# Optimization experiments

Hardware: AMD Instinct MI355X
Metric: run time of the kernel (lower is better)

Reference implementation:

```python
import jax, jax.numpy as jnp
import numpy as np

B, S, HID = 1, 2048, 2048
NH = 16
QL, KVL = 1536, 512
DN, DR, DV = 128, 64, 128
DQ = DN + DR  # 192
IH, ID = 4, 128
TOPK = 1024
EPS = 1e-6
THETA = 10000.0


def rope_interleaved(x, cos, sin):
    # x: (b,s,h,d); cos/sin: (s,d//2); pairs are (x[...,2i], x[...,2i+1])
    xr = x[..., 0::2]
    xi = x[..., 1::2]
    c = cos[None, :, None, :]
    s = sin[None, :, None, :]
    yr = xr * c - xi * s
    yi = xr * s + xi * c
    return jnp.stack([yr, yi], axis=-1).reshape(x.shape)


def rope_noninterleaved(x, cos, sin):
    # rotate-half style: pairs are (x[...,i], x[...,i+d/2])
    d = x.shape[-1] // 2
    x1, x2 = x[..., :d], x[..., d:]
    c = cos[None, :, None, :]
    s = sin[None, :, None, :]
    return jnp.concatenate([x1 * c - x2 * s, x1 * s + x2 * c], axis=-1)


def rmsnorm(x, w):
    var = jnp.mean(x * x, axis=-1, keepdims=True)
    return w * (x * jax.lax.rsqrt(var + EPS))


def layernorm(x, g, b):
    mu = jnp.mean(x, axis=-1, keepdims=True)
    var = jnp.mean((x - mu) ** 2, axis=-1, keepdims=True)
    return (x - mu) * jax.lax.rsqrt(var + EPS) * g + b


def setup_inputs() -> dict:
    key = jax.random.key(0)
    ks = jax.random.split(key, 12)
    std = 0.02
    x = jax.random.normal(ks[0], (B, S, HID), jnp.float32)
    pos = jnp.arange(S, dtype=jnp.float32)
    inv_freq = THETA ** (-jnp.arange(0, DR, 2, dtype=jnp.float32) / DR)
    ang = pos[:, None] * inv_freq[None, :]  # (S, DR//2)
    cos, sin = jnp.cos(ang), jnp.sin(ang)
    mask = jnp.where(jnp.tril(jnp.ones((S, S), bool)), 0.0, -1e9).astype(jnp.float32)
    return {
        "x": x, "cos": cos, "sin": sin, "mask": mask,
        "Wq_a": jax.random.normal(ks[1], (HID, QL), jnp.float32) * std,
        "q_norm_w": jnp.ones((QL,), jnp.float32),
        "Wq_b": jax.random.normal(ks[2], (QL, NH * DQ), jnp.float32) * std,
        "Wkv_a": jax.random.normal(ks[3], (HID, KVL + DR), jnp.float32) * std,
        "kv_norm_w": jnp.ones((KVL,), jnp.float32),
        "Wkv_b": jax.random.normal(ks[4], (KVL, NH * (DN + DV)), jnp.float32) * std,
        "Wo": jax.random.normal(ks[5], (NH * DV, HID), jnp.float32) * std,
        "IWq_b": jax.random.normal(ks[6], (QL, IH * ID), jnp.float32) * std,
        "IWk": jax.random.normal(ks[7], (HID, ID), jnp.float32) * std,
        "Ik_norm_w": jnp.ones((ID,), jnp.float32),
        "Ik_norm_b": jnp.zeros((ID,), jnp.float32),
        "IWproj": jax.random.normal(ks[8], (HID, IH), jnp.float32) * std,
    }


def indexer(x, qr, cos, sin, mask, IWq_b, IWk, Ik_norm_w, Ik_norm_b, IWproj):
    b, s, _ = x.shape
    q = (qr @ IWq_b).reshape(b, s, IH, ID)
    q_pe, q_nope = q[..., :DR], q[..., DR:]
    q_pe = rope_noninterleaved(q_pe, cos, sin)
    q = jnp.concatenate([q_pe, q_nope], axis=-1)
    k = layernorm(x @ IWk, Ik_norm_w, Ik_norm_b)  # (b,s,ID)
    k_pe = rope_noninterleaved(k[:, :, None, :DR], cos, sin)[:, :, 0]
    k = jnp.concatenate([k_pe, k[..., DR:]], axis=-1)
    weights = (x @ IWproj) * (IH ** -0.5) * (ID ** -0.5)  # (b,s,IH)
    logits = jax.nn.relu(jnp.einsum('bthd,bsd->btsh', q, k))
    index_score = jnp.einsum('btsh,bth->bts', logits, weights)
    index_score = index_score + mask[None]
    k_top = min(TOPK, s)
    topk_idx = jax.lax.top_k(index_score, k_top)[1]  # (b,s,k)
    bi = jnp.arange(b)[:, None, None]
    si = jnp.arange(s)[None, :, None]
    index_mask = jnp.full((b, s, s), -1e9, jnp.float32).at[bi, si, topk_idx].set(0.0)
    return index_mask


def reference(x, cos, sin, mask, Wq_a, q_norm_w, Wq_b, Wkv_a, kv_norm_w, Wkv_b, Wo,
              IWq_b, IWk, Ik_norm_w, Ik_norm_b, IWproj):
    b, s, _ = x.shape
    qr = rmsnorm(x @ Wq_a, q_norm_w)  # (b,s,QL)
    q = (qr @ Wq_b).reshape(b, s, NH, DQ)
    q_nope, q_pe = q[..., :DN], q[..., DN:]
    q_pe = rope_interleaved(q_pe, cos, sin)
    q = jnp.concatenate([q_nope, q_pe], axis=-1)
    kv_full = x @ Wkv_a
    kv, k_pe = kv_full[..., :KVL], kv_full[..., KVL:]
    kv = rmsnorm(kv, kv_norm_w)
    k_pe = rope_interleaved(k_pe[:, :, None, :], cos, sin)  # (b,s,1,DR)
    kv_exp = (kv @ Wkv_b).reshape(b, s, NH, DN + DV)
    k_nope, v = kv_exp[..., :DN], kv_exp[..., DN:]
    k = jnp.concatenate([k_nope, jnp.broadcast_to(k_pe, (b, s, NH, DR))], axis=-1)
    scores = jnp.einsum('bshd,bthd->bsht', q, k) * (DQ ** -0.5)
    index_mask = indexer(x, qr, cos, sin, mask, IWq_b, IWk, Ik_norm_w, Ik_norm_b, IWproj)
    scores = scores + index_mask[:, :, None, :] + mask[None, :, None, :]
    probs = jax.nn.softmax(scores, axis=-1)
    out = jnp.einsum('bsht,bthd->bshd', probs, v).reshape(b, s, NH * DV)
    return out @ Wo
```

## Files before the change

### kernel.cpp

```cpp
#include <hip/hip_runtime.h>
#include <math.h>
#include <stdint.h>

#define S 2048
#define HID 2048
#define NH 16
#define QL 1536
#define KVL 512
#define DN 128
#define DR 64
#define DV 128
#define DQ 192
#define IH 4
#define ID 128
#define TOPK 1024

#define N1 2244
#define N2 3584

#define CDIV(a,b) (((a)+(b)-1)/(b))

typedef float f32x4 __attribute__((ext_vector_type(4)));
typedef short bf16x8 __attribute__((ext_vector_type(8)));

__device__ __forceinline__ ushort f2b(float f) {
    uint32_t u = __float_as_uint(f);
    u += 0x7fffu + ((u >> 16) & 1u);
    return (ushort)(u >> 16);
}

#define GLL16(g, l)                                                            \
    __builtin_amdgcn_global_load_lds(                                          \
        (const __attribute__((address_space(1))) void*)(g),                    \
        (__attribute__((address_space(3))) void*)(l), 16, 0, 0)

__global__ __launch_bounds__(256) void gemm_bt(const ushort* __restrict__ A,
                                               const ushort* __restrict__ BT,
                                               float* __restrict__ C,
                                               int M, int N, int K) {
    __shared__ ushort As[2][128 * 32];
    __shared__ ushort Bs[2][128 * 32];
    const int tid = threadIdx.x;
    const int w = tid >> 6, l = tid & 63;
    const int quad = l >> 4, lane = l & 15;
    const int row0 = blockIdx.y * 128, col0 = blockIdx.x * 128;
    const int wr = (w >> 1) * 64, wc = (w & 1) * 64;
    f32x4 acc[4][4];
#pragma unroll
    for (int i = 0; i < 4; i++)
#pragma unroll
        for (int j = 0; j < 4; j++) acc[i][j] = (f32x4)0.f;

    const int srow = w * 32 + (l >> 2);
    const int c8 = (l & 3) * 8;
    const ushort* pa0 = A + (size_t)(row0 + srow) * K + c8;
    const ushort* pa1 = A + (size_t)(row0 + srow + 16) * K + c8;
    int bn0 = col0 + srow;      if (bn0 > N - 1) bn0 = N - 1;
    int bn1 = col0 + srow + 16; if (bn1 > N - 1) bn1 = N - 1;
    const ushort* pb0 = BT + (size_t)bn0 * K + c8;
    const ushort* pb1 = BT + (size_t)bn1 * K + c8;
    const int soff = srow * 32 + c8;

    GLL16(pa0, &As[0][soff]);
    GLL16(pa1, &As[0][soff + 16 * 32]);
    GLL16(pb0, &Bs[0][soff]);
    GLL16(pb1, &Bs[0][soff + 16 * 32]);
    asm volatile("s_waitcnt vmcnt(0)" ::: "memory");
    __builtin_amdgcn_s_barrier();

    int cur = 0;
    for (int k0 = 0; k0 < K; k0 += 32) {
        const int nxt = cur ^ 1;
        if (k0 + 32 < K) {
            GLL16(pa0 + k0 + 32, &As[nxt][soff]);
            GLL16(pa1 + k0 + 32, &As[nxt][soff + 16 * 32]);
            GLL16(pb0 + k0 + 32, &Bs[nxt][soff]);
            GLL16(pb1 + k0 + 32, &Bs[nxt][soff + 16 * 32]);
        }
        bf16x8 af[4], bf[4];
#pragma unroll
        for (int mi = 0; mi < 4; mi++)
            af[mi] = *(const bf16x8*)(&As[cur][(wr + mi * 16 + lane) * 32 + quad * 8]);
#pragma unroll
        for (int ni = 0; ni < 4; ni++)
            bf[ni] = *(const bf16x8*)(&Bs[cur][(wc + ni * 16 + lane) * 32 + quad * 8]);
#pragma unroll
        for (int mi = 0; mi < 4; mi++)
#pragma unroll
            for (int ni = 0; ni < 4; ni++)
                acc[mi][ni] = __builtin_amdgcn_mfma_f32_16x16x32_bf16(af[mi], bf[ni], acc[mi][ni], 0, 0, 0);
        asm volatile("s_waitcnt vmcnt(0)" ::: "memory");
        __builtin_amdgcn_s_barrier();
        cur = nxt;
    }
#pragma unroll
    for (int mi = 0; mi < 4; mi++)
#pragma unroll
        for (int ni = 0; ni < 4; ni++)
#pragma unroll
            for (int r = 0; r < 4; r++) {
                int row = row0 + wr + mi * 16 + quad * 4 + r;
                int col = col0 + wc + ni * 16 + lane;
                if (col < N) C[(size_t)row * N + col] = acc[mi][ni][r];
            }
}

__global__ __launch_bounds__(256) void gemm_bt_h(const ushort* __restrict__ A,
                                                 const ushort* __restrict__ BT,
                                                 ushort* __restrict__ C,
                                                 int M, int N, int K) {
    __shared__ ushort As[2][128 * 32];
    __shared__ ushort Bs[2][128 * 32];
    const int tid = threadIdx.x;
    const int w = tid >> 6, l = tid & 63;
    const int quad = l >> 4, lane = l & 15;
    const int row0 = blockIdx.y * 128, col0 = blockIdx.x * 128;
    const int wr = (w >> 1) * 64, wc = (w & 1) * 64;
    f32x4 acc[4][4];
#pragma unroll
    for (int i = 0; i < 4; i++)
#pragma unroll
        for (int j = 0; j < 4; j++) acc[i][j] = (f32x4)0.f;

    const int srow = w * 32 + (l >> 2);
    const int c8 = (l & 3) * 8;
    const ushort* pa0 = A + (size_t)(row0 + srow) * K + c8;
    const ushort* pa1 = A + (size_t)(row0 + srow + 16) * K + c8;
    int bn0 = col0 + srow;      if (bn0 > N - 1) bn0 = N - 1;
    int bn1 = col0 + srow + 16; if (bn1 > N - 1) bn1 = N - 1;
    const ushort* pb0 = BT + (size_t)bn0 * K + c8;
    const ushort* pb1 = BT + (size_t)bn1 * K + c8;
    const int soff = srow * 32 + c8;

    GLL16(pa0, &As[0][soff]);
    GLL16(pa1, &As[0][soff + 16 * 32]);
    GLL16(pb0, &Bs[0][soff]);
    GLL16(pb1, &Bs[0][soff + 16 * 32]);
    asm volatile("s_waitcnt vmcnt(0)" ::: "memory");
    __builtin_amdgcn_s_barrier();

    int cur = 0;
    for (int k0 = 0; k0 < K; k0 += 32) {
        const int nxt = cur ^ 1;
        if (k0 + 32 < K) {
            GLL16(pa0 + k0 + 32, &As[nxt][soff]);
            GLL16(pa1 + k0 + 32, &As[nxt][soff + 16 * 32]);
            GLL16(pb0 + k0 + 32, &Bs[nxt][soff]);
            GLL16(pb1 + k0 + 32, &Bs[nxt][soff + 16 * 32]);
        }
        bf16x8 af[4], bf[4];
#pragma unroll
        for (int mi = 0; mi < 4; mi++)
            af[mi] = *(const bf16x8*)(&As[cur][(wr + mi * 16 + lane) * 32 + quad * 8]);
#pragma unroll
        for (int ni = 0; ni < 4; ni++)
            bf[ni] = *(const bf16x8*)(&Bs[cur][(wc + ni * 16 + lane) * 32 + quad * 8]);
#pragma unroll
        for (int mi = 0; mi < 4; mi++)
#pragma unroll
            for (int ni = 0; ni < 4; ni++)
                acc[mi][ni] = __builtin_amdgcn_mfma_f32_16x16x32_bf16(af[mi], bf[ni], acc[mi][ni], 0, 0, 0);
        asm volatile("s_waitcnt vmcnt(0)" ::: "memory");
        __builtin_amdgcn_s_barrier();
        cur = nxt;
    }
#pragma unroll
    for (int mi = 0; mi < 4; mi++)
#pragma unroll
        for (int ni = 0; ni < 4; ni++)
#pragma unroll
            for (int r = 0; r < 4; r++) {
                int row = row0 + wr + mi * 16 + quad * 4 + r;
                int col = col0 + wc + ni * 16 + lane;
                if (col < N) C[(size_t)row * N + col] = f2b(acc[mi][ni][r]);
            }
}

__device__ __forceinline__ void wtrans_body(const float* W, ushort* WT, int K, int N,
                                            int k0, int n0) {
    __shared__ float t[64][65];
    int rr = threadIdx.x >> 6, cc = threadIdx.x & 63;
#pragma unroll
    for (int p = 0; p < 16; p++) {
        int k = k0 + p * 4 + rr, n = n0 + cc;
        t[p * 4 + rr][cc] = (k < K && n < N) ? W[(size_t)k * N + n] : 0.f;
    }
    __syncthreads();
#pragma unroll
    for (int p = 0; p < 16; p++) {
        int n = n0 + p * 4 + rr, k = k0 + cc;
        if (n < N && k < K) WT[(size_t)n * K + k] = f2b(t[cc][p * 4 + rr]);
    }
}

__global__ __launch_bounds__(256) void wtrans(const float* __restrict__ W, ushort* __restrict__ WT,
                                              int K, int N) {
    wtrans_body(W, WT, K, N, blockIdx.x * 64, blockIdx.y * 64);
}

__global__ __launch_bounds__(256) void wtrans_c1(const float* __restrict__ W0, const float* __restrict__ W1,
                                                 const float* __restrict__ W2, const float* __restrict__ W3,
                                                 ushort* __restrict__ WT) {
    int yb = blockIdx.y;
    const float* W; int N; size_t off; int y;
    if (yb < 24)      { W = W0; N = 1536; off = 0;                      y = yb; }
    else if (yb < 33) { W = W1; N = 576;  off = (size_t)1536 * HID;     y = yb - 24; }
    else if (yb < 35) { W = W2; N = 128;  off = (size_t)2112 * HID;     y = yb - 33; }
    else              { W = W3; N = 4;    off = (size_t)2240 * HID;     y = yb - 35; }
    wtrans_body(W, WT + off, HID, N, blockIdx.x * 64, y * 64);
}

__global__ __launch_bounds__(256) void wtrans_c2(const float* __restrict__ W0, const float* __restrict__ W1,
                                                 ushort* __restrict__ WT) {
    int yb = blockIdx.y;
    const float* W; int N; size_t off; int y;
    if (yb < 48) { W = W0; N = 3072; off = 0;                  y = yb; }
    else         { W = W1; N = 512;  off = (size_t)3072 * QL;  y = yb - 48; }
    wtrans_body(W, WT + off, QL, N, blockIdx.x * 64, y * 64);
}

__global__ void cvt_bf16(const float* __restrict__ in, ushort* __restrict__ out) {
    int i = blockIdx.x * 256 + threadIdx.x;
    float4 v = *(const float4*)(in + (size_t)i * 4);
    uint32_t lo = (uint32_t)f2b(v.x) | ((uint32_t)f2b(v.y) << 16);
    uint32_t hi = (uint32_t)f2b(v.z) | ((uint32_t)f2b(v.w) << 16);
    *(uint2*)(out + (size_t)i * 4) = make_uint2(lo, hi);
}

__global__ __launch_bounds__(256) void post_c1(const float* __restrict__ C1,
                                               const float* __restrict__ qw,
                                               const float* __restrict__ kvw,
                                               const float* __restrict__ ikg,
                                               const float* __restrict__ ikb,
                                               const float* __restrict__ cosb,
                                               const float* __restrict__ sinb,
                                               ushort* __restrict__ qrb,
                                               ushort* __restrict__ kvnb,
                                               float* __restrict__ kpe,
                                               float* __restrict__ kiT) {
    const int t = blockIdx.x, tid = threadIdx.x;
    const float* row = C1 + (size_t)t * N1;
    __shared__ float red[256];
    __shared__ float kis[128];
    float ss = 0.f;
    for (int i = tid; i < 1536; i += 256) { float v = row[i]; ss += v * v; }
    red[tid] = ss; __syncthreads();
    for (int st = 128; st > 0; st >>= 1) { if (tid < st) red[tid] += red[tid + st]; __syncthreads(); }
    float sq = rsqrtf(red[0] / 1536.f + 1e-6f);
    __syncthreads();
    float s2 = 0.f;
    for (int i = tid; i < 512; i += 256) { float v = row[1536 + i]; s2 += v * v; }
    red[tid] = s2; __syncthreads();
    for (int st = 128; st > 0; st >>= 1) { if (tid < st) red[tid] += red[tid + st]; __syncthreads(); }
    float skv = rsqrtf(red[0] / 512.f + 1e-6f);
    __syncthreads();
    float kv_ = (tid < 128) ? row[2112 + tid] : 0.f;
    red[tid] = kv_; __syncthreads();
    for (int st = 128; st > 0; st >>= 1) { if (tid < st) red[tid] += red[tid + st]; __syncthreads(); }
    float mu = red[0] / 128.f;
    __syncthreads();
    red[tid] = kv_ * kv_; __syncthreads();
    for (int st = 128; st > 0; st >>= 1) { if (tid < st) red[tid] += red[tid + st]; __syncthreads(); }
    float var = red[0] / 128.f - mu * mu;
    for (int i = tid; i < 1536; i += 256) qrb[(size_t)t * QL + i] = f2b(row[i] * sq * qw[i]);
    for (int i = tid; i < 512; i += 256)  kvnb[(size_t)t * KVL + i] = f2b(row[1536 + i] * skv * kvw[i]);
    if (tid < 32) {
        float c = cosb[t * 32 + tid], s = sinb[t * 32 + tid];
        float xr = row[2048 + 2 * tid], xi = row[2048 + 2 * tid + 1];
        kpe[t * 64 + 2 * tid]     = xr * c - xi * s;
        kpe[t * 64 + 2 * tid + 1] = xr * s + xi * c;
    }
    if (tid < 128) kis[tid] = (kv_ - mu) * rsqrtf(var + 1e-6f) * ikg[tid] + ikb[tid];
    __syncthreads();
    if (tid < 128) {
        float outv;
        if (tid < 32) {
            float c = cosb[t * 32 + tid], s = sinb[t * 32 + tid];
            outv = kis[tid] * c - kis[tid + 32] * s;
        } else if (tid < 64) {
            int j = tid - 32;
            float c = cosb[t * 32 + j], s = sinb[t * 32 + j];
            outv = kis[j] * s + kis[tid] * c;
        } else {
            outv = kis[tid];
        }
        kiT[(size_t)tid * S + t] = outv;
    }
}

__global__ __launch_bounds__(256) void post_c2(float* __restrict__ C2,
                                               const float* __restrict__ cosb,
                                               const float* __restrict__ sinb,
                                               ushort* __restrict__ qb) {
    const int t = blockIdx.x, tid = threadIdx.x;
    __shared__ float cs[32], sn[32];
    if (tid < 32) { cs[tid] = cosb[t * 32 + tid]; sn[tid] = sinb[t * 32 + tid]; }
    __syncthreads();
    const float sc = 0.10412775370051047f;
    const float* src0 = C2 + (size_t)t * N2;
    for (int i = tid; i < NH * 96; i += 256) {
        int h = i / 96, p = i % 96;
        const float* src = src0 + h * 192;
        ushort* dst = qb + ((size_t)h * S + t) * 192;
        if (p < 64) {
            dst[2 * p]     = f2b(src[2 * p] * sc);
            dst[2 * p + 1] = f2b(src[2 * p + 1] * sc);
        } else {
            int j = p - 64;
            float c = cs[j], s = sn[j];
            float xr = src[128 + 2 * j], xi = src[128 + 2 * j + 1];
            dst[128 + 2 * j]     = f2b((xr * c - xi * s) * sc);
            dst[128 + 2 * j + 1] = f2b((xr * s + xi * c) * sc);
        }
    }
    if (tid < 128) {
        int h = tid >> 5, j = tid & 31;
        float* p = C2 + (size_t)t * N2 + 3072 + h * 128;
        float c = cs[j], s = sn[j];
        float x1 = p[j], x2 = p[j + 32];
        p[j] = x1 * c - x2 * s;
        p[j + 32] = x1 * s + x2 * c;
    }
}

__global__ __launch_bounds__(256) void pack_kv(const ushort* __restrict__ kvexp_h,
                                               const float* __restrict__ kpe,
                                               ushort* __restrict__ kb,
                                               ushort* __restrict__ vT) {
    __shared__ ushort t[64][136];
    const int s0 = blockIdx.x * 64, h = blockIdx.y, tid = threadIdx.x;
    const int row = tid >> 2, c = tid & 3;
    const ushort* src = kvexp_h + (size_t)(s0 + row) * 4096 + h * 256;
    ushort* kbr = kb + ((size_t)h * S + s0 + row) * 192;
#pragma unroll
    for (int i = 0; i < 4; i++) {
        int off = c * 32 + i * 8;
        *(uint4*)(kbr + off) = *(const uint4*)(src + off);
        *(uint4*)(&t[row][off]) = *(const uint4*)(src + 128 + off);
    }
    const float* kp = kpe + (size_t)(s0 + row) * 64 + c * 16;
#pragma unroll
    for (int i = 0; i < 16; i++) kbr[128 + c * 16 + i] = f2b(kp[i]);
    __syncthreads();
    const int d = tid >> 1, sh = (tid & 1) * 32;
    ushort* dst = vT + ((size_t)h * 128 + d) * S + s0 + sh;
#pragma unroll
    for (int i = 0; i < 32; i++) dst[i] = t[sh + i][d];
}

__global__ __launch_bounds__(256) void iscore4(const float* __restrict__ qi,
                                               const float* __restrict__ kiT,
                                               const float* __restrict__ iw,
                                               float* __restrict__ iscore) {
    int t = blockIdx.x;
    int s0 = blockIdx.y * 1024;
    if (s0 > t) return;
    int s = s0 + threadIdx.x * 4;
    __shared__ float qs[4 * ID];
    __shared__ float ws4[4];
    for (int i = threadIdx.x; i < 4 * ID; i += 256) qs[i] = qi[(size_t)t * N2 + i];
    if (threadIdx.x < 4) ws4[threadIdx.x] = iw[(size_t)t * N1 + threadIdx.x] * 0.04419417382415922f;
    __syncthreads();
    if (s > t) return;
    float a[4][4];
#pragma unroll
    for (int h = 0; h < 4; h++)
#pragma unroll
        for (int c = 0; c < 4; c++) a[h][c] = 0.f;
    for (int d = 0; d < ID; d++) {
        float4 kv = *(const float4*)(kiT + (size_t)d * S + s);
#pragma unroll
        for (int h = 0; h < 4; h++) {
            float qv = qs[h * ID + d];
            a[h][0] += qv * kv.x; a[h][1] += qv * kv.y;
            a[h][2] += qv * kv.z; a[h][3] += qv * kv.w;
        }
    }
#pragma unroll
    for (int c = 0; c < 4; c++) {
        if (s + c > t) break;
        float sc = fmaxf(a[0][c], 0.f) * ws4[0] + fmaxf(a[1][c], 0.f) * ws4[1] +
                   fmaxf(a[2][c], 0.f) * ws4[2] + fmaxf(a[3][c], 0.f) * ws4[3];
        iscore[(size_t)t * S + s + c] = sc;
    }
}

__device__ inline unsigned sortable_u32(float f) {
    unsigned u = __float_as_uint(f);
    return (u & 0x80000000u) ? ~u : (u | 0x80000000u);
}

__global__ __launch_bounds__(256) void topk_mask(const float* __restrict__ iscore,
                                                 uint32_t* __restrict__ msk) {
    int t = blockIdx.x, tid = threadIdx.x;
    uint32_t* mrow = msk + (size_t)t * 64;
    if (t < TOPK) {
        if (tid < 64) {
            int full = (t + 1) >> 5;
            uint32_t wv2 = (tid < full) ? 0xFFFFFFFFu : 0u;
            if (tid == full) { int rem = (t + 1) & 31; wv2 = rem ? ((1u << rem) - 1u) : 0u; }
            mrow[tid] = wv2;
        }
        return;
    }
    const float* row = iscore + (size_t)t * S;
    const int n = t + 1;
    const int wv = tid >> 6;
    __shared__ int hist[4][256];
    __shared__ int scan[256];
    __shared__ int bsel, ksel;
    __shared__ uint32_t bytes[256];

    int jb = tid * 8;
    float4 v0 = *(const float4*)(row + jb);
    float4 v1 = *(const float4*)(row + jb + 4);
    uint32_t lsu[8];
    {
        float vvv[8] = {v0.x, v0.y, v0.z, v0.w, v1.x, v1.y, v1.z, v1.w};
#pragma unroll
        for (int i = 0; i < 8; i++)
            lsu[i] = (jb + i < n) ? sortable_u32(vvv[i]) : 0u;
    }
    unsigned prefix = 0, prefmask = 0;
    int k = TOPK;
    for (int pass = 0; pass < 4; pass++) {
        int shift = 24 - pass * 8;
#pragma unroll
        for (int r = 0; r < 4; r++) hist[r][tid] = 0;
        __syncthreads();
#pragma unroll
        for (int i = 0; i < 8; i++) {
            uint32_t u = lsu[i];
            if ((u & prefmask) == prefix) atomicAdd(&hist[wv][(u >> shift) & 255], 1);
        }
        __syncthreads();
        int h = hist[0][tid] + hist[1][tid] + hist[2][tid] + hist[3][tid];
        scan[tid] = h; __syncthreads();
        for (int st = 1; st < 256; st <<= 1) {
            int a = scan[tid];
            int b = (tid + st < 256) ? scan[tid + st] : 0;
            __syncthreads();
            scan[tid] = a + b;
            __syncthreads();
        }
        int snext = (tid < 255) ? scan[tid + 1] : 0;
        if (scan[tid] >= k && snext < k) { bsel = tid; ksel = k - snext; }
        __syncthreads();
        prefix |= ((unsigned)bsel) << shift;
        prefmask |= 0xFFu << shift;
        k = ksel;
        __syncthreads();
    }
    const unsigned u_thr = prefix;
    const int need = k;
    uint32_t gtbits = 0, eqbits = 0;
    int eqcnt = 0;
#pragma unroll
    for (int i = 0; i < 8; i++) {
        uint32_t u = lsu[i];
        if (u > u_thr) gtbits |= 1u << i;
        else if (u == u_thr) { eqbits |= 1u << i; eqcnt++; }
    }
    scan[tid] = eqcnt; __syncthreads();
    for (int st = 1; st < 256; st <<= 1) {
        int a = scan[tid];
        int b = (tid >= st) ? scan[tid - st] : 0;
        __syncthreads();
        scan[tid] = a + b;
        __syncthreads();
    }
    int room = need - (scan[tid] - eqcnt);
    uint32_t keep = 0;
#pragma unroll
    for (int i = 0; i < 8; i++)
        if ((eqbits >> i) & 1u) { if (room > 0) { keep |= 1u << i; room--; } }
    bytes[tid] = gtbits | keep;
    __syncthreads();
    if (tid < 64)
        mrow[tid] = bytes[tid * 4] | (bytes[tid * 4 + 1] << 8) |
                    (bytes[tid * 4 + 2] << 16) | (bytes[tid * 4 + 3] << 24);
}

__global__ __launch_bounds__(256, 2) void fattn6(const ushort* __restrict__ qb,
                                                 const ushort* __restrict__ kb,
                                                 const ushort* __restrict__ vT,
                                                 const uint32_t* __restrict__ msk,
                                                 float* __restrict__ Opart,
                                                 float* __restrict__ mlbuf) {
    __shared__ ushort Ks[24 * 512];
    __shared__ ushort Vs[16 * 512];
    __shared__ ushort Pm[4][16 * 72];
    const int tid = threadIdx.x;
    const int w = tid >> 6, l = tid & 63, quad = l >> 4, lane = l & 15;
    const int b = blockIdx.x;
    const int r8 = b & 7, j = b >> 3;
    const int h = r8 + 8 * (j & 1);
    const int idx = j >> 1;
    const int pair = idx & 15, part = idx >> 4;
    const int ta = pair, tb = 31 - pair, nA = ta + 1;
    const int vlo = part * 11, vhi = vlo + 11;
    const int qa0 = ta * 64, qb0 = tb * 64;

    bf16x8 qfa[6], qfb[6];
    {
        const ushort* qpa = qb + ((size_t)h * S + qa0 + w * 16 + lane) * 192;
        const ushort* qpb = qb + ((size_t)h * S + qb0 + w * 16 + lane) * 192;
#pragma unroll
        for (int ks = 0; ks < 6; ks++) {
            qfa[ks] = *(const bf16x8*)(qpa + ks * 32 + quad * 8);
            qfb[ks] = *(const bf16x8*)(qpb + ks * 32 + quad * 8);
        }
    }
    f32x4 oa[8], ob[8];
#pragma unroll
    for (int i = 0; i < 8; i++) { oa[i] = (f32x4)0.f; ob[i] = (f32x4)0.f; }
    float ma[4], la[4], mb[4], lb[4];
#pragma unroll
    for (int r = 0; r < 4; r++) { ma[r] = -1e30f; la[r] = 0.f; mb[r] = -1e30f; lb[r] = 0.f; }

    ushort* pw = &Pm[w][0];
    const ushort* kbase = kb + (size_t)h * S * 192;
    const ushort* vbase = vT + (size_t)h * 128 * S;

    for (int kt = 0; kt <= tb; kt++) {
        const int idxB = (kt <= ta) ? 2 * kt : kt + nA;
        const int hasA = (kt <= ta);
        const int idxA = 2 * kt + 1;
        const bool doB = (idxB >= vlo && idxB < vhi);
        const bool doA = hasA && (idxA >= vlo && idxA < vhi);
        if (!(doA || doB)) continue;
        const int s0 = kt * 64;
        __syncthreads();
#pragma unroll
        for (int ii = 0; ii < 6; ii++) {
            const int i = w * 6 + ii;
            const int ks = i >> 2, kq = i & 3;
            const ushort* src = kbase + (size_t)(s0 + kq * 16 + lane) * 192 + ks * 32 + quad * 8;
            GLL16(src, Ks + i * 512 + l * 8);
        }
#pragma unroll
        for (int ii = 0; ii < 4; ii++) {
            const int i = w * 4 + ii;
            const int k2 = i >> 3, nt = i & 7;
            const ushort* src = vbase + (size_t)(nt * 16 + lane) * S + s0 + k2 * 32 + quad * 8;
            GLL16(src, Vs + i * 512 + l * 8);
        }
        __syncthreads();

#pragma unroll
        for (int pass = 0; pass < 2; pass++) {
            if (pass == 0 && !doA) continue;
            if (pass == 1 && !doB) continue;
            const bf16x8* qf = (pass == 0) ? qfa : qfb;
            f32x4* oacc      = (pass == 0) ? oa : ob;
            float* mm        = (pass == 0) ? ma : mb;
            float* ll        = (pass == 0) ? la : lb;
            const int q0t    = (pass == 0) ? qa0 : qb0;

            f32x4 sc[4];
#pragma unroll
            for (int kq = 0; kq < 4; kq++) {
                sc[kq] = (f32x4)0.f;
#pragma unroll
                for (int ks = 0; ks < 6; ks++) {
                    bf16x8 bfr = *(const bf16x8*)(Ks + (ks * 4 + kq) * 512 + quad * 128 + lane * 8);
                    sc[kq] = __builtin_amdgcn_mfma_f32_16x16x32_bf16(qf[ks], bfr, sc[kq], 0, 0, 0);
                }
            }
            uint32_t w0[4], w1[4];
            {
                const int rowbase = q0t + w * 16 + quad * 4;
#pragma unroll
                for (int r = 0; r < 4; r++) {
                    const uint32_t* mp = msk + (size_t)(rowbase + r) * 64 + (s0 >> 5);
                    w0[r] = mp[0]; w1[r] = mp[1];
                }
            }
            float vmax[4] = {-1e30f, -1e30f, -1e30f, -1e30f};
#pragma unroll
            for (int kq = 0; kq < 4; kq++) {
                const int sh = (kq & 1) * 16 + lane;
#pragma unroll
                for (int r = 0; r < 4; r++) {
                    uint32_t word = (kq < 2) ? w0[r] : w1[r];
                    float v = ((word >> sh) & 1u) ? sc[kq][r] : -1e30f;
                    sc[kq][r] = v;
                    vmax[r] = fmaxf(vmax[r], v);
                }
            }
#pragma unroll
            for (int off = 1; off < 16; off <<= 1)
#pragma unroll
                for (int r = 0; r < 4; r++)
                    vmax[r] = fmaxf(vmax[r], __shfl_xor(vmax[r], off, 64));
            float alpha[4], psum[4];
#pragma unroll
            for (int r = 0; r < 4; r++) {
                float mnew = fmaxf(mm[r], vmax[r]);
                alpha[r] = exp2f(mm[r] - mnew);
                mm[r] = mnew;
                psum[r] = 0.f;
            }
#pragma unroll
            for (int kq = 0; kq < 4; kq++)
#pragma unroll
                for (int r = 0; r < 4; r++) {
                    float v = sc[kq][r];
                    float e = (v < -1e29f) ? 0.f : exp2f(v - mm[r]);
                    psum[r] += e;
                    pw[(quad * 4 + r) * 72 + kq * 16 + lane] = f2b(e);
                }
#pragma unroll
            for (int off = 1; off < 16; off <<= 1)
#pragma unroll
                for (int r = 0; r < 4; r++)
                    psum[r] += __shfl_xor(psum[r], off, 64);
#pragma unroll
            for (int r = 0; r < 4; r++) ll[r] = ll[r] * alpha[r] + psum[r];

            bf16x8 pfr[2];
#pragma unroll
            for (int k2 = 0; k2 < 2; k2++)
                pfr[k2] = *(const bf16x8*)(pw + lane * 72 + k2 * 32 + quad * 8);
#pragma unroll
            for (int nt = 0; nt < 8; nt++) {
#pragma unroll
                for (int r = 0; r < 4; r++) oacc[nt][r] *= alpha[r];
#pragma unroll
                for (int k2 = 0; k2 < 2; k2++) {
                    bf16x8 vfr = *(const bf16x8*)(Vs + ((k2 * 8 + nt) * 4 + quad) * 128 + lane * 8);
                    oacc[nt] = __builtin_amdgcn_mfma_f32_16x16x32_bf16(pfr[k2], vfr, oacc[nt], 0, 0, 0);
                }
            }
        }
    }
#pragma unroll
    for (int pass = 0; pass < 2; pass++) {
        const f32x4* oacc = (pass == 0) ? oa : ob;
        const float* mm   = (pass == 0) ? ma : mb;
        const float* ll   = (pass == 0) ? la : lb;
        const int qt      = (pass == 0) ? ta : tb;
        float* Op = Opart + (size_t)((qt * 16 + h) * 3 + part) * (64 * 128);
        float* mlp = mlbuf + (size_t)((qt * 16 + h) * 3 + part) * 128;
#pragma unroll
        for (int nt = 0; nt < 8; nt++)
#pragma unroll
            for (int r = 0; r < 4; r++)
                Op[(w * 16 + quad * 4 + r) * 128 + nt * 16 + lane] = oacc[nt][r];
        if (lane == 0) {
#pragma unroll
            for (int r = 0; r < 4; r++) {
                mlp[(w * 16 + quad * 4 + r) * 2 + 0] = mm[r];
                mlp[(w * 16 + quad * 4 + r) * 2 + 1] = ll[r];
            }
        }
    }
}

__global__ __launch_bounds__(256) void attn_combine(const float* __restrict__ Opart,
                                                    const float* __restrict__ mlbuf,
                                                    ushort* __restrict__ attn_b) {
    const int qt = blockIdx.x, h = blockIdx.y, tid = threadIdx.x;
    const size_t base = ((size_t)qt * 16 + h) * 3;
    const float* Op0 = Opart + base * 8192;
    const float* Op1 = Op0 + 8192;
    const float* Op2 = Op1 + 8192;
    const float* ml0 = mlbuf + base * 128;
    const float* ml1 = ml0 + 128;
    const float* ml2 = ml1 + 128;
#pragma unroll
    for (int i = 0; i < 32; i++) {
        int id = tid + i * 256;
        int row = id >> 7, d = id & 127;
        float m0 = ml0[row * 2], l0 = ml0[row * 2 + 1];
        float m1 = ml1[row * 2], l1 = ml1[row * 2 + 1];
        float m2 = ml2[row * 2], l2 = ml2[row * 2 + 1];
        float m = fmaxf(fmaxf(m0, m1), m2);
        float e0 = exp2f(m0 - m), e1 = exp2f(m1 - m), e2 = exp2f(m2 - m);
        float linv = 1.f / (l0 * e0 + l1 * e1 + l2 * e2);
        float v = (Op0[id] * e0 + Op1[id] * e1 + Op2[id] * e2) * linv;
        attn_b[(size_t)(qt * 64 + row) * 2048 + h * 128 + d] = f2b(v);
    }
}

extern "C" void kernel_launch(void* const* d_in, const int* in_sizes, int n_in,
                              void* d_out, int out_size, void* d_ws, size_t ws_size,
                              hipStream_t stream) {
    const float* x        = (const float*)d_in[0];
    const float* cosb     = (const float*)d_in[1];
    const float* sinb     = (const float*)d_in[2];
    const float* Wq_a     = (const float*)d_in[4];
    const float* q_norm_w = (const float*)d_in[5];
    const float* Wq_b     = (const float*)d_in[6];
    const float* Wkv_a    = (const float*)d_in[7];
    const float* kv_norm_w= (const float*)d_in[8];
    const float* Wkv_b    = (const float*)d_in[9];
    const float* Wo       = (const float*)d_in[10];
    const float* IWq_b    = (const float*)d_in[11];
    const float* IWk      = (const float*)d_in[12];
    const float* Ik_norm_w= (const float*)d_in[13];
    const float* Ik_norm_b= (const float*)d_in[14];
    const float* IWproj   = (const float*)d_in[15];
    float* out = (float*)d_out;

    char* ws = (char*)d_ws;
    size_t o = 0;
    auto take = [&](size_t b) { char* p = ws + o; o += (b + 255) & ~(size_t)255; return p; };
    ushort* xb     = (ushort*)take((size_t)S * HID * 2);
    ushort* qrb    = (ushort*)take((size_t)S * QL * 2);
    ushort* qb     = (ushort*)take((size_t)NH * S * DQ * 2);
    ushort* kvnb   = (ushort*)take((size_t)S * KVL * 2);
    float*  kpe    = (float*)take((size_t)S * DR * 4);
    ushort* kb     = (ushort*)take((size_t)NH * S * DQ * 2);
    ushort* vT     = (ushort*)take((size_t)NH * DV * S * 2);
    uint32_t* msk  = (uint32_t*)take((size_t)S * 64 * 4);
    float*  mlbuf  = (float*)take((size_t)32 * 16 * 3 * 64 * 2 * 4);
    ushort* WTp    = (ushort*)take((size_t)N2 * QL * 2);
    float*  C1     = (float*)take((size_t)S * N1 * 4);
    char*   big    = take((size_t)32 * 16 * 3 * 8192 * 4 + 1024);
    ushort* kvexp_h= (ushort*)take((size_t)S * 4096 * 2);
    float*  kiT    = (float*)take((size_t)128 * S * 4);
    char*   poolb  = take((size_t)16777216);

    float* C2     = (float*)big;
    float* Opart  = (float*)big;
    float* iscore = (float*)poolb;
    ushort* attn_b = (ushort*)poolb;

    cvt_bf16<<<(S * HID) / 1024, 256, 0, stream>>>(x, xb);

    wtrans_c1<<<dim3(32, 36), 256, 0, stream>>>(Wq_a, Wkv_a, IWk, IWproj, WTp);
    gemm_bt<<<dim3(CDIV(N1, 128), S / 128), 256, 0, stream>>>(xb, WTp, C1, S, N1, HID);
    post_c1<<<S, 256, 0, stream>>>(C1, q_norm_w, kv_norm_w, Ik_norm_w, Ik_norm_b,
                                   cosb, sinb, qrb, kvnb, kpe, kiT);

    wtrans_c2<<<dim3(24, 56), 256, 0, stream>>>(Wq_b, IWq_b, WTp);
    gemm_bt<<<dim3(N2 / 128, S / 128), 256, 0, stream>>>(qrb, WTp, C2, S, N2, QL);
    post_c2<<<S, 256, 0, stream>>>(C2, cosb, sinb, qb);

    wtrans<<<dim3(8, 64), 256, 0, stream>>>(Wkv_b, WTp, KVL, NH * (DN + DV));
    gemm_bt_h<<<dim3(32, S / 128), 256, 0, stream>>>(kvnb, WTp, kvexp_h, S, NH * (DN + DV), KVL);
    pack_kv<<<dim3(S / 64, NH), 256, 0, stream>>>(kvexp_h, kpe, kb, vT);

    iscore4<<<dim3(S, S / 1024), 256, 0, stream>>>(C2 + 3072, kiT, C1 + 2240, iscore);
    topk_mask<<<S, 256, 0, stream>>>(iscore, msk);

    fattn6<<<768, 256, 0, stream>>>(qb, kb, vT, msk, Opart, mlbuf);
    attn_combine<<<dim3(32, 16), 256, 0, stream>>>(Opart, mlbuf, attn_b);

    wtrans<<<dim3(32, 32), 256, 0, stream>>>(Wo, WTp, NH * DV, HID);
    gemm_bt<<<dim3(HID / 128, S / 128), 256, 0, stream>>>(attn_b, WTp, out, S, HID, NH * DV);

    (void)in_sizes; (void)n_in; (void)out_size; (void)ws_size; (void)o;
}
```

Before: 514.9 us.

## Deepen GEMM K-tile to 64 with XOR-swizzled LDS layout

Both bf16 GEMM kernels now stage 64-wide K tiles instead of 32, halving the number of barrier/wait iterations per output tile. LDS rows are XOR-swizzled by row index, at source-address computation and at fragment read time, to avoid bank conflicts on the 128-byte row stride. LDS use doubles to 64 KB per block, which may reduce occupancy. The code assumes K is a multiple of 64.

```diff
diff --git a/kernel.cpp b/kernel.cpp
--- a/kernel.cpp
+++ b/kernel.cpp
@@ -38,8 +38,8 @@
                                                const ushort* __restrict__ BT,
                                                float* __restrict__ C,
                                                int M, int N, int K) {
-    __shared__ ushort As[2][128 * 32];
-    __shared__ ushort Bs[2][128 * 32];
+    __shared__ ushort As[2][128 * 64];
+    __shared__ ushort Bs[2][128 * 64];
     const int tid = threadIdx.x;
     const int w = tid >> 6, l = tid & 63;
     const int quad = l >> 4, lane = l & 15;
@@ -51,47 +51,55 @@
 #pragma unroll
         for (int j = 0; j < 4; j++) acc[i][j] = (f32x4)0.f;
 
-    const int srow = w * 32 + (l >> 2);
-    const int c8 = (l & 3) * 8;
-    const ushort* pa0 = A + (size_t)(row0 + srow) * K + c8;
-    const ushort* pa1 = A + (size_t)(row0 + srow + 16) * K + c8;
-    int bn0 = col0 + srow;      if (bn0 > N - 1) bn0 = N - 1;
-    int bn1 = col0 + srow + 16; if (bn1 > N - 1) bn1 = N - 1;
-    const ushort* pb0 = BT + (size_t)bn0 * K + c8;
-    const ushort* pb1 = BT + (size_t)bn1 * K + c8;
-    const int soff = srow * 32 + c8;
-
-    GLL16(pa0, &As[0][soff]);
-    GLL16(pa1, &As[0][soff + 16 * 32]);
-    GLL16(pb0, &Bs[0][soff]);
-    GLL16(pb1, &Bs[0][soff + 16 * 32]);
+    const int r32 = tid >> 3;
+    const int csw = (((tid & 7) ^ (r32 & 7)) * 8);
+    const ushort* pA[4];
+    const ushort* pB[4];
+#pragma unroll
+    for (int p = 0; p < 4; p++) {
+        pA[p] = A + (size_t)(row0 + p * 32 + r32) * K + csw;
+        int bn = col0 + p * 32 + r32; if (bn > N - 1) bn = N - 1;
+        pB[p] = BT + (size_t)bn * K + csw;
+    }
+    const int doff = r32 * 64 + (tid & 7) * 8;
+
+#define STG64(k0, s)                                                           \
+    {                                                                          \
+        _Pragma("unroll")                                                      \
+        for (int p = 0; p < 4; p++) {                                          \
+            GLL16(pA[p] + (k0), &As[s][p * 2048 + doff]);                      \
+            GLL16(pB[p] + (k0), &Bs[s][p * 2048 + doff]);                      \
+        }                                                                      \
+    }
+
+    const int nt = K >> 6;
+    STG64(0, 0);
     asm volatile("s_waitcnt vmcnt(0)" ::: "memory");
     __builtin_amdgcn_s_barrier();
 
+    const int xsw = (lane & 7) << 3;
     int cur = 0;
-    for (int k0 = 0; k0 < K; k0 += 32) {
-        const int nxt = cur ^ 1;
-        if (k0 + 32 < K) {
-            GLL16(pa0 + k0 + 32, &As[nxt][soff]);
-            GLL16(pa1 + k0 + 32, &As[nxt][soff + 16 * 32]);
-            GLL16(pb0 + k0 + 32, &Bs[nxt][soff]);
-            GLL16(pb1 + k0 + 32, &Bs[nxt][soff + 16 * 32]);
-        }
-        bf16x8 af[4], bf[4];
-#pragma unroll
-        for (int mi = 0; mi < 4; mi++)
-            af[mi] = *(const bf16x8*)(&As[cur][(wr + mi * 16 + lane) * 32 + quad * 8]);
-#pragma unroll
-        for (int ni = 0; ni < 4; ni++)
-            bf[ni] = *(const bf16x8*)(&Bs[cur][(wc + ni * 16 + lane) * 32 + quad * 8]);
-#pragma unroll
-        for (int mi = 0; mi < 4; mi++)
+    for (int t = 0; t < nt; ++t) {
+        if (t + 1 < nt) STG64((t + 1) * 64, cur ^ 1);
+#pragma unroll
+        for (int kk = 0; kk < 2; kk++) {
+            const int fo = (kk * 32 + quad * 8) ^ xsw;
+            bf16x8 af[4], bf[4];
+#pragma unroll
+            for (int mi = 0; mi < 4; mi++)
+                af[mi] = *(const bf16x8*)(&As[cur][(wr + mi * 16 + lane) * 64 + fo]);
 #pragma unroll
             for (int ni = 0; ni < 4; ni++)
-                acc[mi][ni] = __builtin_amdgcn_mfma_f32_16x16x32_bf16(af[mi], bf[ni], acc[mi][ni], 0, 0, 0);
+                bf[ni] = *(const bf16x8*)(&Bs[cur][(wc + ni * 16 + lane) * 64 + fo]);
+#pragma unroll
+            for (int mi = 0; mi < 4; mi++)
+#pragma unroll
+                for (int ni = 0; ni < 4; ni++)
+                    acc[mi][ni] = __builtin_amdgcn_mfma_f32_16x16x32_bf16(af[mi], bf[ni], acc[mi][ni], 0, 0, 0);
+        }
         asm volatile("s_waitcnt vmcnt(0)" ::: "memory");
         __builtin_amdgcn_s_barrier();
-        cur = nxt;
+        cur ^= 1;
     }
 #pragma unroll
     for (int mi = 0; mi < 4; mi++)
@@ -109,8 +117,8 @@
                                                  const ushort* __restrict__ BT,
                                                  ushort* __restrict__ C,
                                                  int M, int N, int K) {
-    __shared__ ushort As[2][128 * 32];
-    __shared__ ushort Bs[2][128 * 32];
+    __shared__ ushort As[2][128 * 64];
+    __shared__ ushort Bs[2][128 * 64];
     const int tid = threadIdx.x;
     const int w = tid >> 6, l = tid & 63;
     const int quad = l >> 4, lane = l & 15;
@@ -122,47 +130,46 @@
 #pragma unroll
         for (int j = 0; j < 4; j++) acc[i][j] = (f32x4)0.f;
 
-    const int srow = w * 32 + (l >> 2);
-    const int c8 = (l & 3) * 8;
-    const ushort* pa0 = A + (size_t)(row0 + srow) * K + c8;
-    const ushort* pa1 = A + (size_t)(row0 + srow + 16) * K + c8;
-    int bn0 = col0 + srow;      if (bn0 > N - 1) bn0 = N - 1;
-    int bn1 = col0 + srow + 16; if (bn1 > N - 1) bn1 = N - 1;
-    const ushort* pb0 = BT + (size_t)bn0 * K + c8;
-    const ushort* pb1 = BT + (size_t)bn1 * K + c8;
-    const int soff = srow * 32 + c8;
-
-    GLL16(pa0, &As[0][soff]);
-    GLL16(pa1, &As[0][soff + 16 * 32]);
-    GLL16(pb0, &Bs[0][soff]);
-    GLL16(pb1, &Bs[0][soff + 16 * 32]);
+    const int r32 = tid >> 3;
+    const int csw = (((tid & 7) ^ (r32 & 7)) * 8);
+    const ushort* pA[4];
+    const ushort* pB[4];
+#pragma unroll
+    for (int p = 0; p < 4; p++) {
+        pA[p] = A + (size_t)(row0 + p * 32 + r32) * K + csw;
+        int bn = col0 + p * 32 + r32; if (bn > N - 1) bn = N - 1;
+        pB[p] = BT + (size_t)bn * K + csw;
+    }
+    const int doff = r32 * 64 + (tid & 7) * 8;
+
+    const int nt = K >> 6;
+    STG64(0, 0);
     asm volatile("s_waitcnt vmcnt(0)" ::: "memory");
     __builtin_amdgcn_s_barrier();
 
+    const int xsw = (lane & 7) << 3;
     int cur = 0;
-    for (int k0 = 0; k0 < K; k0 += 32) {
-        const int nxt = cur ^ 1;
-        if (k0 + 32 < K) {
-            GLL16(pa0 + k0 + 32, &As[nxt][soff]);
-            GLL16(pa1 + k0 + 32, &As[nxt][soff + 16 * 32]);
-            GLL16(pb0 + k0 + 32, &Bs[nxt][soff]);
-            GLL16(pb1 + k0 + 32, &Bs[nxt][soff + 16 * 32]);
-        }
-        bf16x8 af[4], bf[4];
-#pragma unroll
-        for (int mi = 0; mi < 4; mi++)
-            af[mi] = *(const bf16x8*)(&As[cur][(wr + mi * 16 + lane) * 32 + quad * 8]);
-#pragma unroll
-        for (int ni = 0; ni < 4; ni++)
-            bf[ni] = *(const bf16x8*)(&Bs[cur][(wc + ni * 16 + lane) * 32 + quad * 8]);
-#pragma unroll
-        for (int mi = 0; mi < 4; mi++)
+    for (int t = 0; t < nt; ++t) {
+        if (t + 1 < nt) STG64((t + 1) * 64, cur ^ 1);
+#pragma unroll
+        for (int kk = 0; kk < 2; kk++) {
+            const int fo = (kk * 32 + quad * 8) ^ xsw;
+            bf16x8 af[4], bf[4];
+#pragma unroll
+            for (int mi = 0; mi < 4; mi++)
+                af[mi] = *(const bf16x8*)(&As[cur][(wr + mi * 16 + lane) * 64 + fo]);
 #pragma unroll
             for (int ni = 0; ni < 4; ni++)
-                acc[mi][ni] = __builtin_amdgcn_mfma_f32_16x16x32_bf16(af[mi], bf[ni], acc[mi][ni], 0, 0, 0);
+                bf[ni] = *(const bf16x8*)(&Bs[cur][(wc + ni * 16 + lane) * 64 + fo]);
+#pragma unroll
+            for (int mi = 0; mi < 4; mi++)
+#pragma unroll
+                for (int ni = 0; ni < 4; ni++)
+                    acc[mi][ni] = __builtin_amdgcn_mfma_f32_16x16x32_bf16(af[mi], bf[ni], acc[mi][ni], 0, 0, 0);
+        }
         asm volatile("s_waitcnt vmcnt(0)" ::: "memory");
         __builtin_amdgcn_s_barrier();
-        cur = nxt;
+        cur ^= 1;
     }
 #pragma unroll
     for (int mi = 0; mi < 4; mi++)
```

New measurement: 496.6 us. -3.6%, faster.
